# Kernel tuning notes

Hardware: AMD Instinct MI355X
Metric: run time of the kernel (lower is better)

## Reference

```python
import jax, jax.numpy as jnp
import numpy as np

BLOCK = 9      # photometric_loss block size
LOSS_EPS = 0.5 # census ternary threshold


def _sign_eps(d, eps):
    # ternary census: -1 / 0 / +1 with dead-zone eps
    return jnp.where(d < -eps, -1.0, jnp.where(d > eps, 1.0, 0.0))


def _census_sad(es, ta, block, eps):
    # per-pixel mean over valid 9x9 window of |census(es) - census(ta)|
    B, C, H, W = es.shape
    P = block // 2
    pad = ((0, 0), (0, 0), (P, P), (P, P))
    esp = jnp.pad(es, pad)
    tap = jnp.pad(ta, pad)
    vp = jnp.pad(jnp.ones((1, 1, H, W), es.dtype), pad)  # validity of shifted px
    total = jnp.zeros_like(es)
    count = jnp.zeros((1, 1, H, W), es.dtype)
    for dh in range(-P, P + 1):          # fixed 9x9 structural loop
        for dw in range(-P, P + 1):
            es_s = esp[:, :, P + dh:P + dh + H, P + dw:P + dw + W]
            ta_s = tap[:, :, P + dh:P + dh + H, P + dw:P + dw + W]
            v = vp[:, :, P + dh:P + dh + H, P + dw:P + dw + W]
            c = jnp.abs(_sign_eps(es_s - es, eps) - _sign_eps(ta_s - ta, eps))
            total = total + v * c
            count = count + v
    return total / count


def reference(disp0, im, pattern):
    B, _, H, W = disp0.shape
    # pattern.mean(dim=1, keepdim=True)
    pat = jnp.broadcast_to(pattern.mean(axis=1, keepdims=True), (B, 1, H, W))
    # grid_sample(align_corners=True, border) with y unchanged reduces to
    # clamped 1D linear interpolation along width at x = u - disp
    u = jnp.arange(W, dtype=disp0.dtype)
    x = jnp.clip(u[None, None, None, :] - disp0, 0.0, W - 1)  # [B,1,H,W]
    x0 = jnp.floor(x).astype(jnp.int32)
    x1 = jnp.minimum(x0 + 1, W - 1)
    w = x - x0.astype(x.dtype)
    p0 = jnp.take_along_axis(pat, x0, axis=3)
    p1 = jnp.take_along_axis(pat, x1, axis=3)
    pattern_proj = p0 * (1.0 - w) + p1 * w
    diff = _census_sad(pattern_proj, im, BLOCK, LOSS_EPS)
    # mask = ones (std=None): (mask*diff).sum()/mask.sum() == mean
    val = diff.mean()
    return val, pattern_proj


def setup_inputs() -> dict:
    key = jax.random.key(0)
    k1, k2, k3 = jax.random.split(key, 3)
    B, H, W = 16, 512, 640
    disp0 = jax.random.uniform(k1, (B, 1, H, W), dtype=jnp.float32) * 64.0
    im = jax.random.uniform(k2, (B, 1, H, W), dtype=jnp.float32)
    pattern = jax.random.uniform(k3, (1, 3, H, W), dtype=jnp.float32)
    return {"disp0": disp0, "im": im, "pattern": pattern}
```

## Files before the change

kernel.cpp:

```cpp
#include <hip/hip_runtime.h>

#define BB 16
#define HH 512
#define WW 640
constexpr int HW = HH * WW;

#define WT 64
#define HT 16
#define RP 4
#define PAD 4
#define LW (WT + 2*PAD)
#define LH (HT + PAD)
#define GX (WW / WT)
#define GY (HH / HT)
#define NBLK (GX * GY * BB)

constexpr float HALO = 1.0e6f;

__device__ __forceinline__ float fast_rcp(float x) {
    return __builtin_amdgcn_rcpf(x);
}

__device__ __forceinline__ float census_interior(const float* es_t, const float* ta_t,
                                                 int tx, int rg)
{
    float ehi[RP], elo[RP], thi[RP], tlo[RP];
    #pragma unroll
    for (int p = 0; p < RP; ++p) {
        int lr = rg * RP + p;
        float ec = es_t[lr * LW + tx + PAD];
        float tc = ta_t[lr * LW + tx + PAD];
        ehi[p] = ec + 0.5f;  elo[p] = ec - 0.5f;
        thi[p] = tc + 0.5f;  tlo[p] = tc - 0.5f;
    }

    int acca[RP] = {0, 0, 0, 0};
    int accb[RP] = {0, 0, 0, 0};

    #pragma unroll
    for (int wr = 0; wr < RP + PAD; ++wr) {
        const int lr = rg * RP + wr;
        float e[9], t[9];
        #pragma unroll
        for (int j = 0; j < 9; ++j) {
            e[j] = es_t[lr * LW + tx + j];
            t[j] = ta_t[lr * LW + tx + j];
        }
        if (wr < RP) {
            #pragma unroll
            for (int j = 5; j <= 8; ++j) {
                acca[wr] += (int)((e[j] > ehi[wr]) != (t[j] > thi[wr]));
                accb[wr] += (int)((e[j] < elo[wr]) != (t[j] < tlo[wr]));
            }
        }
        #pragma unroll
        for (int p = 0; p < RP; ++p) {
            if (p <= wr - 1 && p >= wr - PAD) {
                #pragma unroll
                for (int j = 0; j <= 8; ++j) {
                    acca[p] += (int)((e[j] > ehi[p]) != (t[j] > thi[p]));
                    accb[p] += (int)((e[j] < elo[p]) != (t[j] < tlo[p]));
                }
            }
        }
    }
    int acc = (acca[0] + acca[1]) + (acca[2] + acca[3])
            + (accb[0] + accb[1]) + (accb[2] + accb[3]);
    return (float)acc;
}

__device__ __forceinline__ float census_edge(const float* es_t, const float* ta_t,
                                             int tx, int rg, int bx, int by)
{
    float invcw[9];
    const int w0 = bx * WT + tx;
    #pragma unroll
    for (int j = 0; j < 9; ++j) {
        int c  = w0 + j - PAD;
        int cw = min(PAD, WW - 1 - c) + min(PAD, c) + 1;
        invcw[j] = fast_rcp((float)cw);
    }
    float rowinv[RP + PAD];
    #pragma unroll
    for (int wr = 0; wr < RP + PAD; ++wr) {
        int r  = by * HT + rg * RP + wr;
        int ch = min(PAD, HH - 1 - r) + min(PAD, r) + 1;
        rowinv[wr] = fast_rcp((float)ch);
    }

    float ec[RP], tc[RP], wp[RP], facc[RP];
    #pragma unroll
    for (int p = 0; p < RP; ++p) {
        int lr = rg * RP + p;
        ec[p] = es_t[lr * LW + tx + PAD];
        tc[p] = ta_t[lr * LW + tx + PAD];
        wp[p] = rowinv[p] * invcw[PAD];
        facc[p] = 0.0f;
    }

    #pragma unroll
    for (int wr = 0; wr < RP + PAD; ++wr) {
        const int lr = rg * RP + wr;
        float e[9], t[9];
        #pragma unroll
        for (int j = 0; j < 9; ++j) {
            e[j] = es_t[lr * LW + tx + j];
            t[j] = ta_t[lr * LW + tx + j];
        }
        #pragma unroll
        for (int p = 0; p < RP; ++p) {
            const bool d0 = (p == wr);
            if (p <= wr && p >= wr - PAD) {
                #pragma unroll
                for (int j = 0; j <= 8; ++j) {
                    if (d0 && j <= 4) continue;
                    float s1 = rintf(__builtin_amdgcn_fmed3f(e[j] - ec[p], -1.0f, 1.0f));
                    float s2 = rintf(__builtin_amdgcn_fmed3f(t[j] - tc[p], -1.0f, 1.0f));
                    float c  = fabsf(s1 - s2);
                    float wt = fmaf(rowinv[wr], invcw[j], wp[p]);
                    facc[p] = fmaf(c, wt, facc[p]);
                }
            }
        }
    }
    return (facc[0] + facc[1]) + (facc[2] + facc[3]);
}

__global__ __launch_bounds__(256)
void fused_kernel(const float* __restrict__ disp0,
                  const float* __restrict__ im,
                  const float* __restrict__ pattern,
                  float* __restrict__ out,
                  float* __restrict__ partial)
{
    __shared__ float es_t[LH * LW];
    __shared__ float ta_t[LH * LW];
    __shared__ float wsum[4];

    const int bx = blockIdx.x, by = blockIdx.y, b = blockIdx.z;
    const int tx = threadIdx.x;
    const int rg = threadIdx.y;
    const int tid = rg * 64 + tx;

    const float* db = disp0 + (size_t)b * HW;
    const float* ib = im    + (size_t)b * HW;
    float* proj = out + 1 + (size_t)b * HW;

    const int gh0 = by * HT;
    const int gw0 = bx * WT - PAD;

    #pragma unroll
    for (int it = 0; it < (LH * LW + 255) / 256; ++it) {
        int i = tid + it * 256;
        if (i < LH * LW) {
            int lh = i / LW;
            int lw = i - lh * LW;
            int gh = gh0 + lh, gw = gw0 + lw;
            float ev = HALO, tv = HALO;
            if ((gh < HH) & (gw >= 0) & (gw < WW)) {
                int g = gh * WW + gw;
                float d = db[g];
                float x = fminf(fmaxf((float)gw - d, 0.0f), (float)(WW - 1));
                int   x0 = (int)x;
                int   x1 = min(x0 + 1, WW - 1);
                float w  = x - (float)x0;
                const float* prow = pattern + gh * WW;
                float p0 = (prow[x0] + prow[HW + x0] + prow[2*HW + x0]) * (1.0f/3.0f);
                float p1 = (prow[x1] + prow[HW + x1] + prow[2*HW + x1]) * (1.0f/3.0f);
                ev = p0 * (1.0f - w) + p1 * w;
                tv = ib[g];
                if ((lh < HT) & (lw >= PAD) & (lw < PAD + WT))
                    proj[g] = ev;
            }
            es_t[i] = ev;
            ta_t[i] = tv;
        }
    }
    __syncthreads();

    float tsum;
    if ((bx >= 1) & (bx <= GX - 2) & (by >= 1) & (by <= GY - 2)) {
        tsum = census_interior(es_t, ta_t, tx, rg) * (2.0f / 81.0f);
    } else {
        tsum = census_edge(es_t, ta_t, tx, rg, bx, by);
    }

    #pragma unroll
    for (int off = 32; off > 0; off >>= 1)
        tsum += __shfl_down(tsum, off, 64);
    if (tx == 0) wsum[rg] = tsum;
    __syncthreads();
    if (tid == 0)
        partial[(b * GY + by) * GX + bx] = wsum[0] + wsum[1] + wsum[2] + wsum[3];
}

__global__ __launch_bounds__(256)
void reduce_kernel(const float* __restrict__ partial, float* __restrict__ out)
{
    __shared__ float wsum[4];
    int t = threadIdx.x;
    float s = 0.0f;
    #pragma unroll
    for (int i = 0; i < NBLK / 256; ++i) s += partial[t + i * 256];
    #pragma unroll
    for (int off = 32; off > 0; off >>= 1)
        s += __shfl_down(s, off, 64);
    if ((t & 63) == 0) wsum[t >> 6] = s;
    __syncthreads();
    if (t == 0)
        out[0] = (wsum[0] + wsum[1] + wsum[2] + wsum[3]) * (1.0f / ((float)BB * (float)HW));
}

extern "C" void kernel_launch(void* const* d_in, const int* in_sizes, int n_in,
                              void* d_out, int out_size, void* d_ws, size_t ws_size,
                              hipStream_t stream) {
    const float* disp0   = (const float*)d_in[0];
    const float* im      = (const float*)d_in[1];
    const float* pattern = (const float*)d_in[2];
    float* out = (float*)d_out;
    float* partial = (float*)d_ws;

    dim3 grid(GX, GY, BB);
    dim3 block(64, 4);
    fused_kernel<<<grid, block, 0, stream>>>(disp0, im, pattern, out, partial);
    reduce_kernel<<<1, 256, 0, stream>>>(partial, out);
}
```

Before: 171.2 us.

## Precompute pattern mean, interleave smem as float2, use ballot-popcount census

Adds a pre-pass kernel that averages the three pattern channels once, so the fused kernel does two gathers instead of six per pixel. Shared memory becomes interleaved float2 (estimate, target) so each neighbour needs a single LDS load. The interior census counts mismatches with wavefront ballots and popcount rather than per-lane integer accumulation, which also removes the shuffle reduction. The edge path splits its weight into a per-neighbour part and a per-center part folded in at the end. Loads are hoisted ahead of the compute loop and the launch bound asks for 6 blocks per CU; the extra launch and wider ballot work per compare are the costs taken on.

```diff
diff --git a/kernel.cpp b/kernel.cpp
--- a/kernel.cpp
+++ b/kernel.cpp
@@ -11,6 +11,8 @@
 #define PAD 4
 #define LW (WT + 2*PAD)
 #define LH (HT + PAD)
+#define LHW (LH * LW)
+#define NIT ((LHW + 255) / 256)
 #define GX (WW / WT)
 #define GY (HH / HT)
 #define NBLK (GX * GY * BB)
@@ -21,56 +23,54 @@
     return __builtin_amdgcn_rcpf(x);
 }
 
-__device__ __forceinline__ float census_interior(const float* es_t, const float* ta_t,
-                                                 int tx, int rg)
+__global__ __launch_bounds__(256)
+void pm_kernel(const float* __restrict__ pattern, float* __restrict__ pm)
+{
+    int i = blockIdx.x * 256 + threadIdx.x;
+    if (i < HW)
+        pm[i] = (pattern[i] + pattern[HW + i] + pattern[2 * HW + i]) * (1.0f / 3.0f);
+}
+
+__device__ __forceinline__ unsigned census_interior(const float2* sm, int tx, int rg)
 {
     float ehi[RP], elo[RP], thi[RP], tlo[RP];
     #pragma unroll
     for (int p = 0; p < RP; ++p) {
-        int lr = rg * RP + p;
-        float ec = es_t[lr * LW + tx + PAD];
-        float tc = ta_t[lr * LW + tx + PAD];
-        ehi[p] = ec + 0.5f;  elo[p] = ec - 0.5f;
-        thi[p] = tc + 0.5f;  tlo[p] = tc - 0.5f;
-    }
-
-    int acca[RP] = {0, 0, 0, 0};
-    int accb[RP] = {0, 0, 0, 0};
-
+        float2 c = sm[(rg * RP + p) * LW + tx + PAD];
+        ehi[p] = c.x + 0.5f;  elo[p] = c.x - 0.5f;
+        thi[p] = c.y + 0.5f;  tlo[p] = c.y - 0.5f;
+    }
+    unsigned acc = 0;
     #pragma unroll
     for (int wr = 0; wr < RP + PAD; ++wr) {
-        const int lr = rg * RP + wr;
-        float e[9], t[9];
-        #pragma unroll
-        for (int j = 0; j < 9; ++j) {
-            e[j] = es_t[lr * LW + tx + j];
-            t[j] = ta_t[lr * LW + tx + j];
-        }
-        if (wr < RP) {
-            #pragma unroll
-            for (int j = 5; j <= 8; ++j) {
-                acca[wr] += (int)((e[j] > ehi[wr]) != (t[j] > thi[wr]));
-                accb[wr] += (int)((e[j] < elo[wr]) != (t[j] < tlo[wr]));
-            }
-        }
+        const float2* row = sm + (rg * RP + wr) * LW + tx;
+        float2 v[9];
+        #pragma unroll
+        for (int j = 0; j < 9; ++j) v[j] = row[j];
         #pragma unroll
         for (int p = 0; p < RP; ++p) {
-            if (p <= wr - 1 && p >= wr - PAD) {
+            if (p == wr) {
+                #pragma unroll
+                for (int j = 5; j <= 8; ++j) {
+                    unsigned long long mh = __ballot(v[j].x > ehi[p]) ^ __ballot(v[j].y > thi[p]);
+                    unsigned long long ml = __ballot(v[j].x < elo[p]) ^ __ballot(v[j].y < tlo[p]);
+                    acc += (unsigned)__popcll(mh) + (unsigned)__popcll(ml);
+                }
+            } else if (p >= wr - PAD && p < wr) {
                 #pragma unroll
                 for (int j = 0; j <= 8; ++j) {
-                    acca[p] += (int)((e[j] > ehi[p]) != (t[j] > thi[p]));
-                    accb[p] += (int)((e[j] < elo[p]) != (t[j] < tlo[p]));
+                    unsigned long long mh = __ballot(v[j].x > ehi[p]) ^ __ballot(v[j].y > thi[p]);
+                    unsigned long long ml = __ballot(v[j].x < elo[p]) ^ __ballot(v[j].y < tlo[p]);
+                    acc += (unsigned)__popcll(mh) + (unsigned)__popcll(ml);
                 }
             }
         }
     }
-    int acc = (acca[0] + acca[1]) + (acca[2] + acca[3])
-            + (accb[0] + accb[1]) + (accb[2] + accb[3]);
-    return (float)acc;
-}
-
-__device__ __forceinline__ float census_edge(const float* es_t, const float* ta_t,
-                                             int tx, int rg, int bx, int by)
+    return acc;
+}
+
+__device__ __forceinline__ float census_edge(const float2* sm, int tx, int rg,
+                                             int bx, int by)
 {
     float invcw[9];
     const int w0 = bx * WT + tx;
@@ -80,33 +80,35 @@
         int cw = min(PAD, WW - 1 - c) + min(PAD, c) + 1;
         invcw[j] = fast_rcp((float)cw);
     }
-    float rowinv[RP + PAD];
+
+    float ehi[RP], elo[RP], thi[RP], tlo[RP], wp[RP], facc[RP];
+    int iacc[RP];
+    #pragma unroll
+    for (int p = 0; p < RP; ++p) {
+        float2 c = sm[(rg * RP + p) * LW + tx + PAD];
+        ehi[p] = c.x + 0.5f;  elo[p] = c.x - 0.5f;
+        thi[p] = c.y + 0.5f;  tlo[p] = c.y - 0.5f;
+        int r  = by * HT + rg * RP + p;
+        int ch = min(PAD, HH - 1 - r) + min(PAD, r) + 1;
+        wp[p]  = fast_rcp((float)ch) * invcw[PAD];
+        facc[p] = 0.0f;
+        iacc[p] = 0;
+    }
+
     #pragma unroll
     for (int wr = 0; wr < RP + PAD; ++wr) {
         int r  = by * HT + rg * RP + wr;
         int ch = min(PAD, HH - 1 - r) + min(PAD, r) + 1;
-        rowinv[wr] = fast_rcp((float)ch);
-    }
-
-    float ec[RP], tc[RP], wp[RP], facc[RP];
-    #pragma unroll
-    for (int p = 0; p < RP; ++p) {
-        int lr = rg * RP + p;
-        ec[p] = es_t[lr * LW + tx + PAD];
-        tc[p] = ta_t[lr * LW + tx + PAD];
-        wp[p] = rowinv[p] * invcw[PAD];
-        facc[p] = 0.0f;
-    }
-
-    #pragma unroll
-    for (int wr = 0; wr < RP + PAD; ++wr) {
-        const int lr = rg * RP + wr;
-        float e[9], t[9];
-        #pragma unroll
-        for (int j = 0; j < 9; ++j) {
-            e[j] = es_t[lr * LW + tx + j];
-            t[j] = ta_t[lr * LW + tx + j];
-        }
+        float rowinv = fast_rcp((float)ch);
+        float wq[9];
+        #pragma unroll
+        for (int j = 0; j < 9; ++j) wq[j] = rowinv * invcw[j];
+
+        const float2* row = sm + (rg * RP + wr) * LW + tx;
+        float2 v[9];
+        #pragma unroll
+        for (int j = 0; j < 9; ++j) v[j] = row[j];
+
         #pragma unroll
         for (int p = 0; p < RP; ++p) {
             const bool d0 = (p == wr);
@@ -114,27 +116,30 @@
                 #pragma unroll
                 for (int j = 0; j <= 8; ++j) {
                     if (d0 && j <= 4) continue;
-                    float s1 = rintf(__builtin_amdgcn_fmed3f(e[j] - ec[p], -1.0f, 1.0f));
-                    float s2 = rintf(__builtin_amdgcn_fmed3f(t[j] - tc[p], -1.0f, 1.0f));
-                    float c  = fabsf(s1 - s2);
-                    float wt = fmaf(rowinv[wr], invcw[j], wp[p]);
-                    facc[p] = fmaf(c, wt, facc[p]);
+                    int bh = (int)((v[j].x > ehi[p]) != (v[j].y > thi[p]));
+                    int bl = (int)((v[j].x < elo[p]) != (v[j].y < tlo[p]));
+                    int c  = bh + bl;
+                    facc[p] = fmaf((float)c, wq[j], facc[p]);
+                    iacc[p] += c;
                 }
             }
         }
     }
-    return (facc[0] + facc[1]) + (facc[2] + facc[3]);
-}
-
-__global__ __launch_bounds__(256)
+    float sum = 0.0f;
+    #pragma unroll
+    for (int p = 0; p < RP; ++p)
+        sum += facc[p] + wp[p] * (float)iacc[p];
+    return sum;
+}
+
+__global__ __launch_bounds__(256, 6)
 void fused_kernel(const float* __restrict__ disp0,
                   const float* __restrict__ im,
-                  const float* __restrict__ pattern,
+                  const float* __restrict__ pm,
                   float* __restrict__ out,
                   float* __restrict__ partial)
 {
-    __shared__ float es_t[LH * LW];
-    __shared__ float ta_t[LH * LW];
+    __shared__ float2 sm[LHW];
     __shared__ float wsum[4];
 
     const int bx = blockIdx.x, by = blockIdx.y, b = blockIdx.z;
@@ -149,46 +154,51 @@
     const int gh0 = by * HT;
     const int gw0 = bx * WT - PAD;
 
-    #pragma unroll
-    for (int it = 0; it < (LH * LW + 255) / 256; ++it) {
+    float dv[NIT], tv[NIT];
+    #pragma unroll
+    for (int it = 0; it < NIT; ++it) {
         int i = tid + it * 256;
-        if (i < LH * LW) {
-            int lh = i / LW;
-            int lw = i - lh * LW;
+        int lh = i / LW, lw = i - lh * LW;
+        int gh = gh0 + lh, gw = gw0 + lw;
+        bool ok = (i < LHW) & (gh < HH) & (gw >= 0) & (gw < WW);
+        int g = gh * WW + gw;
+        dv[it] = ok ? db[g] : 0.0f;
+        tv[it] = ok ? ib[g] : HALO;
+    }
+    #pragma unroll
+    for (int it = 0; it < NIT; ++it) {
+        int i = tid + it * 256;
+        if (i < LHW) {
+            int lh = i / LW, lw = i - lh * LW;
             int gh = gh0 + lh, gw = gw0 + lw;
-            float ev = HALO, tv = HALO;
+            float ev = HALO;
             if ((gh < HH) & (gw >= 0) & (gw < WW)) {
                 int g = gh * WW + gw;
-                float d = db[g];
-                float x = fminf(fmaxf((float)gw - d, 0.0f), (float)(WW - 1));
+                float x = fminf(fmaxf((float)gw - dv[it], 0.0f), (float)(WW - 1));
                 int   x0 = (int)x;
                 int   x1 = min(x0 + 1, WW - 1);
                 float w  = x - (float)x0;
-                const float* prow = pattern + gh * WW;
-                float p0 = (prow[x0] + prow[HW + x0] + prow[2*HW + x0]) * (1.0f/3.0f);
-                float p1 = (prow[x1] + prow[HW + x1] + prow[2*HW + x1]) * (1.0f/3.0f);
+                const float* pr = pm + gh * WW;
+                float p0 = pr[x0], p1 = pr[x1];
                 ev = p0 * (1.0f - w) + p1 * w;
-                tv = ib[g];
                 if ((lh < HT) & (lw >= PAD) & (lw < PAD + WT))
                     proj[g] = ev;
             }
-            es_t[i] = ev;
-            ta_t[i] = tv;
+            sm[i] = make_float2(ev, tv[it]);
         }
     }
     __syncthreads();
 
-    float tsum;
     if ((bx >= 1) & (bx <= GX - 2) & (by >= 1) & (by <= GY - 2)) {
-        tsum = census_interior(es_t, ta_t, tx, rg) * (2.0f / 81.0f);
+        unsigned acc = census_interior(sm, tx, rg);
+        if (tx == 0) wsum[rg] = (float)acc * (2.0f / 81.0f);
     } else {
-        tsum = census_edge(es_t, ta_t, tx, rg, bx, by);
-    }
-
-    #pragma unroll
-    for (int off = 32; off > 0; off >>= 1)
-        tsum += __shfl_down(tsum, off, 64);
-    if (tx == 0) wsum[rg] = tsum;
+        float tsum = census_edge(sm, tx, rg, bx, by);
+        #pragma unroll
+        for (int off = 32; off > 0; off >>= 1)
+            tsum += __shfl_down(tsum, off, 64);
+        if (tx == 0) wsum[rg] = tsum;
+    }
     __syncthreads();
     if (tid == 0)
         partial[(b * GY + by) * GX + bx] = wsum[0] + wsum[1] + wsum[2] + wsum[3];
@@ -218,10 +228,13 @@
     const float* im      = (const float*)d_in[1];
     const float* pattern = (const float*)d_in[2];
     float* out = (float*)d_out;
-    float* partial = (float*)d_ws;
+    float* pm      = (float*)d_ws;
+    float* partial = pm + HW;
+
+    pm_kernel<<<(HW + 255) / 256, 256, 0, stream>>>(pattern, pm);
 
     dim3 grid(GX, GY, BB);
     dim3 block(64, 4);
-    fused_kernel<<<grid, block, 0, stream>>>(disp0, im, pattern, out, partial);
+    fused_kernel<<<grid, block, 0, stream>>>(disp0, im, pm, out, partial);
     reduce_kernel<<<1, 256, 0, stream>>>(partial, out);
 }
```

Result: slower. 474.3 us (+177.0%).
